# Kernel optimization log

Hardware: AMD Instinct MI355X
Metric: run time of the kernel (lower is better)

Reference implementation:

```python
import jax, jax.numpy as jnp
import numpy as np

NUM_NODES = 512
HEADS = 4
IN_F = 256
OUT_F = 128
EPS = 1e-5


def _layernorm(x, g, b):
    mu = jnp.mean(x, axis=-1, keepdims=True)
    var = jnp.mean(jnp.square(x - mu), axis=-1, keepdims=True)
    return (x - mu) * jax.lax.rsqrt(var + EPS) * g + b


def setup_inputs() -> dict:
    key = jax.random.key(0)
    ks = jax.random.split(key, 16)
    N = 32 * NUM_NODES
    E = 262144
    s = 0.05
    return {
        "x": jax.random.normal(ks[0], (N, IN_F), jnp.float32),
        "edge_index": jax.random.randint(ks[1], (2, E), 0, N, jnp.int64),
        "W_l": jax.random.normal(ks[2], (IN_F, HEADS * OUT_F), jnp.float32) * s,
        "W_r": jax.random.normal(ks[3], (IN_F, HEADS * OUT_F), jnp.float32) * s,
        "att": jax.random.normal(ks[4], (HEADS, OUT_F), jnp.float32) * s,
        "gat_bias": jnp.zeros((OUT_F,), jnp.float32),
        "gat_gamma": jnp.ones((OUT_F,), jnp.float32),
        "gat_beta": jnp.zeros((OUT_F,), jnp.float32),
        "cnn_W": jax.random.normal(ks[5], (IN_F, OUT_F), jnp.float32) * s,
        "cnn_b": jnp.zeros((OUT_F,), jnp.float32),
        "conv_W": jax.random.normal(ks[6], (OUT_F, OUT_F, 7), jnp.float32) * s,
        "conv_b": jnp.zeros((OUT_F,), jnp.float32),
        "cnn_gamma": jnp.ones((OUT_F,), jnp.float32),
        "cnn_beta": jnp.zeros((OUT_F,), jnp.float32),
        "res_W": jax.random.normal(ks[7], (IN_F, OUT_F), jnp.float32) * s,
        "res_b": jnp.zeros((OUT_F,), jnp.float32),
        "fuse_gamma": jnp.ones((OUT_F,), jnp.float32),
        "fuse_beta": jnp.zeros((OUT_F,), jnp.float32),
    }


def reference(x, edge_index, W_l, W_r, att, gat_bias, gat_gamma, gat_beta,
              cnn_W, cnn_b, conv_W, conv_b, cnn_gamma, cnn_beta,
              res_W, res_b, fuse_gamma, fuse_beta):
    N = x.shape[0]
    B = N // NUM_NODES
    # --- GATv2 branch (add self-loops like PyG default) ---
    loop = jnp.arange(N, dtype=edge_index.dtype)
    src = jnp.concatenate([edge_index[0], loop])
    dst = jnp.concatenate([edge_index[1], loop])
    x_l = (x @ W_l).reshape(N, HEADS, OUT_F)
    x_r = (x @ W_r).reshape(N, HEADS, OUT_F)
    e = x_l[src] + x_r[dst]                      # [E+N, H, F]
    e = jnp.where(e > 0, e, 0.2 * e)             # leaky_relu, slope 0.2
    score = jnp.einsum('ehf,hf->eh', e, att)     # [E+N, H]
    m = jax.ops.segment_max(score, dst, num_segments=N)
    ex = jnp.exp(score - m[dst])
    denom = jax.ops.segment_sum(ex, dst, num_segments=N)
    alpha = ex / denom[dst]
    agg = jax.ops.segment_sum(alpha[:, :, None] * x_l[src], dst, num_segments=N)
    h_gat = jnp.mean(agg, axis=1) + gat_bias     # concat=False -> head mean
    h_gat = jnp.where(h_gat > 0, h_gat, 0.01 * h_gat)  # nn.LeakyReLU default
    h_gat = _layernorm(h_gat, gat_gamma, gat_beta)
    # --- CNN branch ---
    xc = x @ cnn_W + cnn_b                       # [N, F]
    xc = xc.reshape(B, NUM_NODES, OUT_F).transpose(0, 2, 1)  # [B, F, L]
    hc = jax.lax.conv_general_dilated(xc, conv_W, window_strides=(1,),
                                      padding=[(3, 3)],
                                      dimension_numbers=('NCW', 'OIW', 'NCW'))
    hc = hc + conv_b[None, :, None]
    hc = hc.transpose(0, 2, 1).reshape(N, OUT_F)
    hc = jax.nn.relu(hc)
    hc = _layernorm(hc, cnn_gamma, cnn_beta)
    # --- fuse + residual ---
    h = h_gat + hc + (x @ res_W + res_b)
    return _layernorm(h, fuse_gamma, fuse_beta)
```

## Files before the change

kernel.cpp:

```cpp
#include <hip/hip_runtime.h>
#include <hip/hip_bf16.h>
#include <math.h>

#define IN_F 256
#define OUT_F 128
#define HEADS 4
#define HF 512
#define NCAT 1280

typedef __hip_bfloat16 bf16;
typedef unsigned short ushort_t;

using bf16x8 = __attribute__((ext_vector_type(8))) short;
using f32x4  = __attribute__((ext_vector_type(4))) float;
using f32v2  = __attribute__((ext_vector_type(2))) float;

__device__ __forceinline__ float bflo(unsigned u) { return __uint_as_float(u << 16); }
__device__ __forceinline__ float bfhi(unsigned u) { return __uint_as_float(u & 0xffff0000u); }
__device__ __forceinline__ float bf2f(ushort_t u) { return __uint_as_float((unsigned)u << 16); }
__device__ __forceinline__ ushort_t f2bf(float f) {
    __hip_bfloat16 h = __float2bfloat16(f);
    return *reinterpret_cast<ushort_t*>(&h);
}

__device__ __forceinline__ void gload16(const void* g, void* l) {
    __builtin_amdgcn_global_load_lds(
        (const __attribute__((address_space(1))) unsigned int*)g,
        (__attribute__((address_space(3))) unsigned int*)l, 16, 0, 0);
}

template <int CTRL>
__device__ __forceinline__ float dpp_add(float s) {
    int t = __builtin_amdgcn_update_dpp(0, __float_as_int(s), CTRL, 0xf, 0xf, true);
    return s + __int_as_float(t);
}
__device__ __forceinline__ float rowsum16(float s) {
    s = dpp_add<0x121>(s);
    s = dpp_add<0x122>(s);
    s = dpp_add<0x124>(s);
    s = dpp_add<0x128>(s);
    return s;
}

__global__ __launch_bounds__(256) void prep_kernel(
    const float* __restrict__ x, ushort_t* __restrict__ xb, int n_cvt,
    const float* __restrict__ Wl, const float* __restrict__ Wr,
    const float* __restrict__ Wc, const float* __restrict__ Wres,
    const float* __restrict__ Wconv,
    ushort_t* __restrict__ Wt, ushort_t* __restrict__ Wt2,
    const int* __restrict__ ei, int* __restrict__ counts, int E,
    int g1, int g2) {
    int b = blockIdx.x;
    if (b < g1) {
        int i = (b * 256 + threadIdx.x) * 8;
        if (i >= n_cvt) return;
        float4 a = *(const float4*)(x + i);
        float4 c = *(const float4*)(x + i + 4);
        uint4 o;
        o.x = f2bf(a.x) | ((unsigned)f2bf(a.y) << 16);
        o.y = f2bf(a.z) | ((unsigned)f2bf(a.w) << 16);
        o.z = f2bf(c.x) | ((unsigned)f2bf(c.y) << 16);
        o.w = f2bf(c.z) | ((unsigned)f2bf(c.w) << 16);
        *(uint4*)(xb + i) = o;
    } else if (b < g2) {
        int idx = (b - g1) * 256 + threadIdx.x;
        if (idx < NCAT * 256) {
            int n = idx >> 8, k = idx & 255;
            float v;
            if (n < 512)       v = Wl[(size_t)k * 512 + n];
            else if (n < 1024) v = Wr[(size_t)k * 512 + (n - 512)];
            else if (n < 1152) v = Wc[(size_t)k * 128 + (n - 1024)];
            else               v = Wres[(size_t)k * 128 + (n - 1152)];
            Wt[idx] = f2bf(v);
        } else {
            int j = idx - NCAT * 256;
            if (j < 7 * 128 * 128) {
                int k = j >> 14, o = (j >> 7) & 127, i = j & 127;
                Wt2[j] = f2bf(Wconv[((size_t)o * 128 + i) * 7 + k]);
            }
        }
    } else {
        int e = (b - g2) * 256 + threadIdx.x;
        if (e < E) atomicAdd(&counts[ei[E + e]], 1);
    }
}

__global__ __launch_bounds__(256) void mfma_gemm(
    const ushort_t* __restrict__ A,
    const ushort_t* __restrict__ Wt,
    ushort_t* __restrict__ xlb, ushort_t* __restrict__ xrb,
    ushort_t* __restrict__ xcb, ushort_t* __restrict__ resb,
    int M) {
    __shared__ __align__(1024) ushort_t As[128 * 64];
    __shared__ __align__(1024) ushort_t Bs[128 * 64];
    int tid = threadIdx.x;
    int lane = tid & 63, wid = tid >> 6;
    int wr = (wid >> 1) * 64, wc = (wid & 1) * 64;
    int brow = blockIdx.y * 128, bcol = blockIdx.x * 128;
    int srow = lane >> 3;
    int sslot = lane & 7;
    int rl = lane & 15, kq = lane >> 4;
    f32x4 acc[4][4] = {};
    for (int k0 = 0; k0 < 256; k0 += 64) {
        #pragma unroll
        for (int j = 0; j < 4; ++j) {
            int r = (wid * 4 + j) * 8 + srow;
            int sl = sslot ^ (r & 7);
            gload16(A  + (size_t)(brow + r) * 256 + k0 + sl * 8,
                    (char*)As + (wid * 4 + j) * 1024);
            gload16(Wt + (size_t)(bcol + r) * 256 + k0 + sl * 8,
                    (char*)Bs + (wid * 4 + j) * 1024);
        }
        __syncthreads();
        #pragma unroll
        for (int ks = 0; ks < 2; ++ks) {
            int cb = ks * 64 + kq * 16;
            bf16x8 af[4], bfv[4];
            #pragma unroll
            for (int m = 0; m < 4; ++m) {
                int r = wr + m * 16 + rl;
                af[m] = *(const bf16x8*)((const char*)As + r * 128 + (cb ^ ((r & 7) << 4)));
            }
            #pragma unroll
            for (int n = 0; n < 4; ++n) {
                int r = wc + n * 16 + rl;
                bfv[n] = *(const bf16x8*)((const char*)Bs + r * 128 + (cb ^ ((r & 7) << 4)));
            }
            #pragma unroll
            for (int m = 0; m < 4; ++m)
                #pragma unroll
                for (int n = 0; n < 4; ++n)
                    acc[m][n] = __builtin_amdgcn_mfma_f32_16x16x32_bf16(
                        af[m], bfv[n], acc[m][n], 0, 0, 0);
        }
        __syncthreads();
    }
    ushort_t* dstp; int cstride, cb2;
    if (bcol < 512)       { dstp = xlb;  cstride = 512; cb2 = bcol; }
    else if (bcol < 1024) { dstp = xrb;  cstride = 512; cb2 = bcol - 512; }
    else if (bcol < 1152) { dstp = xcb;  cstride = 128; cb2 = bcol - 1024; }
    else                  { dstp = resb; cstride = 128; cb2 = bcol - 1152; }
    int rowb = (lane >> 4) * 4;
    #pragma unroll
    for (int m = 0; m < 4; ++m)
        #pragma unroll
        for (int n = 0; n < 4; ++n) {
            int col = cb2 + wc + n * 16 + rl;
            #pragma unroll
            for (int q = 0; q < 4; ++q) {
                int row = brow + wr + m * 16 + rowb + q;
                dstp[(size_t)row * cstride + col] = f2bf(acc[m][n][q]);
            }
        }
}

__global__ __launch_bounds__(1024) void scan_kernel(
    const int* __restrict__ counts, int* __restrict__ offs,
    int* __restrict__ cursor, int N) {
    __shared__ int wsum[16];
    int t = threadIdx.x;
    int lane = t & 63, w = t >> 6;
    int base = t * 16;
    int local[16], s = 0;
    #pragma unroll
    for (int i = 0; i < 16; ++i) {
        int v = (base + i < N) ? counts[base + i] : 0;
        local[i] = v; s += v;
    }
    int sc = s;
    #pragma unroll
    for (int off = 1; off < 64; off <<= 1) {
        int v = __shfl_up(sc, off);
        if (lane >= off) sc += v;
    }
    if (lane == 63) wsum[w] = sc;
    __syncthreads();
    if (w == 0 && lane < 16) {
        int v = wsum[lane];
        int scv = v;
        #pragma unroll
        for (int off = 1; off < 16; off <<= 1) {
            int u = __shfl_up(scv, off);
            if (lane >= off) scv += u;
        }
        wsum[lane] = scv - v;
    }
    __syncthreads();
    int run = wsum[w] + sc - s;
    #pragma unroll
    for (int i = 0; i < 16; ++i) {
        if (base + i < N) { offs[base + i] = run; cursor[base + i] = run; }
        run += local[i];
    }
}

__global__ __launch_bounds__(256) void scatter_kernel(
    const int* __restrict__ ei, int* __restrict__ cursor,
    int* __restrict__ srcs, int E) {
    int e = blockIdx.x * 256 + threadIdx.x;
    if (e < E) {
        int d = ei[E + e];
        int p = atomicAdd(&cursor[d], 1);
        srcs[p] = ei[e];
    }
}

__global__ __launch_bounds__(256) void conv_ln_kernel(
    const ushort_t* __restrict__ xcb, const float* __restrict__ cnn_b,
    const ushort_t* __restrict__ Wt2, const float* __restrict__ conv_b,
    const float* __restrict__ cnn_gamma, const float* __restrict__ cnn_beta,
    ushort_t* __restrict__ hcn_ln) {
    __shared__ ushort_t As[38][136];
    __shared__ __align__(1024) ushort_t Bs[128 * 128];
    __shared__ float hbuf[32][129];
    int tid = threadIdx.x;
    int lane = tid & 63, wid = tid >> 6;
    int wr = (wid >> 1) * 16, wc = (wid & 1) * 64;
    int b = blockIdx.y, l0 = blockIdx.x * 32;
    for (int u = tid; u < 38 * 16; u += 256) {
        int r = u >> 4, seg = u & 15;
        int l = l0 - 3 + r;
        uint4 o4 = make_uint4(0, 0, 0, 0);
        if (l >= 0 && l < 512) {
            uint4 v = *(const uint4*)(xcb + (size_t)(b * 512 + l) * 128 + seg * 8);
            float4 b0 = *(const float4*)(cnn_b + seg * 8);
            float4 b1 = *(const float4*)(cnn_b + seg * 8 + 4);
            o4.x = f2bf(bflo(v.x) + b0.x) | ((unsigned)f2bf(bfhi(v.x) + b0.y) << 16);
            o4.y = f2bf(bflo(v.y) + b0.z) | ((unsigned)f2bf(bfhi(v.y) + b0.w) << 16);
            o4.z = f2bf(bflo(v.z) + b1.x) | ((unsigned)f2bf(bfhi(v.z) + b1.y) << 16);
            o4.w = f2bf(bflo(v.w) + b1.z) | ((unsigned)f2bf(bfhi(v.w) + b1.w) << 16);
        }
        *(uint4*)&As[r][seg * 8] = o4;
    }
    f32x4 acc[4] = {};
    int rl = lane & 15, kb = (lane >> 4) * 8;
    int sr4 = lane >> 4, ss = lane & 15;
    for (int k = 0; k < 7; ++k) {
        __syncthreads();
        #pragma unroll
        for (int j = 0; j < 8; ++j) {
            int r = (wid * 8 + j) * 4 + sr4;
            int sl = ss ^ (r & 15);
            gload16(Wt2 + ((size_t)(k * 128 + r)) * 128 + sl * 8,
                    (char*)Bs + (wid * 8 + j) * 1024);
        }
        __syncthreads();
        #pragma unroll
        for (int kk = 0; kk < 4; ++kk) {
            bf16x8 af = *(const bf16x8*)&As[wr + rl + k][kk * 32 + kb];
            int cbyte = kk * 64 + (lane >> 4) * 16;
            #pragma unroll
            for (int n = 0; n < 4; ++n) {
                int r = wc + n * 16 + rl;
                bf16x8 bfr = *(const bf16x8*)((const char*)Bs + r * 256
                                              + (cbyte ^ ((r & 15) << 4)));
                acc[n] = __builtin_amdgcn_mfma_f32_16x16x32_bf16(af, bfr, acc[n], 0, 0, 0);
            }
        }
    }
    __syncthreads();
    int rowb = (lane >> 4) * 4;
    #pragma unroll
    for (int n = 0; n < 4; ++n) {
        int col = wc + n * 16 + rl;
        float cb = conv_b[col];
        #pragma unroll
        for (int q = 0; q < 4; ++q) {
            int r = wr + rowb + q;
            hbuf[r][col] = fmaxf(acc[n][q] + cb, 0.f);
        }
    }
    __syncthreads();
    for (int r = wid * 8; r < wid * 8 + 8; ++r) {
        int grow = b * 512 + l0 + r;
        float h0 = hbuf[r][lane], h1 = hbuf[r][lane + 64];
        float s = h0 + h1;
        #pragma unroll
        for (int off = 32; off; off >>= 1) s += __shfl_xor(s, off);
        float mu = s * (1.f / 128.f);
        float d0 = h0 - mu, d1 = h1 - mu;
        float vs = d0 * d0 + d1 * d1;
        #pragma unroll
        for (int off = 32; off; off >>= 1) vs += __shfl_xor(vs, off);
        float inv = rsqrtf(vs * (1.f / 128.f) + 1e-5f);
        size_t base = (size_t)grow * 128;
        hcn_ln[base + lane]      = f2bf(d0 * inv * cnn_gamma[lane]      + cnn_beta[lane]);
        hcn_ln[base + lane + 64] = f2bf(d1 * inv * cnn_gamma[lane + 64] + cnn_beta[lane + 64]);
    }
}

__global__ __launch_bounds__(256) void gat_final_kernel(
    const ushort_t* __restrict__ xlb, const ushort_t* __restrict__ xrb,
    const int* __restrict__ srcs, const int* __restrict__ offs,
    const float* __restrict__ att, const float* __restrict__ gat_bias,
    const float* __restrict__ gat_gamma, const float* __restrict__ gat_beta,
    const ushort_t* __restrict__ hcn_ln, const ushort_t* __restrict__ resb,
    const float* __restrict__ res_b,
    const float* __restrict__ fuse_gamma, const float* __restrict__ fuse_beta,
    float* __restrict__ out, int E, int N) {
    int wid = (blockIdx.x * 256 + threadIdx.x) >> 6;
    int lane = threadIdx.x & 63;
    if (wid >= N) return;
    int d = wid;
    const uint4 rv = ((const uint4*)(xrb + (size_t)d * HF))[lane];
    f32v2 xr2[4];
    xr2[0] = f32v2{bflo(rv.x), bfhi(rv.x)};
    xr2[1] = f32v2{bflo(rv.y), bfhi(rv.y)};
    xr2[2] = f32v2{bflo(rv.z), bfhi(rv.z)};
    xr2[3] = f32v2{bflo(rv.w), bfhi(rv.w)};
    const float LOG2E = 1.44269504f;
    const float4 a0 = ((const float4*)att)[lane * 2];
    const float4 a1 = ((const float4*)att)[lane * 2 + 1];
    f32v2 aw2[4] = {f32v2{a0.x, a0.y} * LOG2E, f32v2{a0.z, a0.w} * LOG2E,
                    f32v2{a1.x, a1.y} * LOG2E, f32v2{a1.z, a1.w} * LOG2E};
    f32v2 acc2[4] = {};
    float dn = 0.f;

    auto process = [&](uint4 lv) {
        f32v2 xl2[4];
        xl2[0] = f32v2{bflo(lv.x), bfhi(lv.x)};
        xl2[1] = f32v2{bflo(lv.y), bfhi(lv.y)};
        xl2[2] = f32v2{bflo(lv.z), bfhi(lv.z)};
        xl2[3] = f32v2{bflo(lv.w), bfhi(lv.w)};
        f32v2 s1 = {0.f, 0.f}, s2 = {0.f, 0.f};
        #pragma unroll
        for (int j = 0; j < 4; ++j) {
            f32v2 v = xl2[j] + xr2[j];
            s1 = __builtin_elementwise_fma(v, aw2[j], s1);
            s2 = __builtin_elementwise_fma(__builtin_elementwise_abs(v), aw2[j], s2);
        }
        float s = fmaf(0.6f, s1.x + s1.y, 0.4f * (s2.x + s2.y));
        s = rowsum16(s);
        float ex = exp2f(s);
        dn += ex;
        f32v2 exv = {ex, ex};
        #pragma unroll
        for (int j = 0; j < 4; ++j)
            acc2[j] = __builtin_elementwise_fma(exv, xl2[j], acc2[j]);
    };

    process(((const uint4*)(xlb + (size_t)d * HF))[lane]);

    int start = offs[d];
    int end = (d == N - 1) ? E : offs[d + 1];
    int p = start;
    for (; p + 3 < end; p += 4) {
        int s0 = srcs[p], s1 = srcs[p + 1], s2 = srcs[p + 2], s3 = srcs[p + 3];
        uint4 l0 = ((const uint4*)(xlb + (size_t)s0 * HF))[lane];
        uint4 l1 = ((const uint4*)(xlb + (size_t)s1 * HF))[lane];
        uint4 l2 = ((const uint4*)(xlb + (size_t)s2 * HF))[lane];
        uint4 l3 = ((const uint4*)(xlb + (size_t)s3 * HF))[lane];
        process(l0); process(l1); process(l2); process(l3);
    }
    for (; p < end; ++p)
        process(((const uint4*)(xlb + (size_t)srcs[p] * HF))[lane]);

    float inv = 1.f / dn;
    float v[8];
    #pragma unroll
    for (int j = 0; j < 4; ++j) {
        float tx = acc2[j].x * inv, ty = acc2[j].y * inv;
        tx += __shfl_xor(tx, 16); tx += __shfl_xor(tx, 32);
        ty += __shfl_xor(ty, 16); ty += __shfl_xor(ty, 32);
        v[2 * j] = tx; v[2 * j + 1] = ty;
    }
    int h = lane >> 4;
    int col = (lane & 15) * 8 + 2 * h;
    float g0 = 0.25f * v[2 * h]     + gat_bias[col];
    float g1 = 0.25f * v[2 * h + 1] + gat_bias[col + 1];
    g0 = g0 > 0.f ? g0 : 0.01f * g0;
    g1 = g1 > 0.f ? g1 : 0.01f * g1;
    float s = g0 + g1;
    #pragma unroll
    for (int off = 32; off; off >>= 1) s += __shfl_xor(s, off);
    float mu = s * (1.f / 128.f);
    float d0 = g0 - mu, d1 = g1 - mu;
    float vs = d0 * d0 + d1 * d1;
    #pragma unroll
    for (int off = 32; off; off >>= 1) vs += __shfl_xor(vs, off);
    float rinv = rsqrtf(vs * (1.f / 128.f) + 1e-5f);
    float hg0 = d0 * rinv * gat_gamma[col]     + gat_beta[col];
    float hg1 = d1 * rinv * gat_gamma[col + 1] + gat_beta[col + 1];
    size_t base = (size_t)d * 128 + col;
    unsigned hcu = *(const unsigned*)(hcn_ln + base);
    unsigned rsu = *(const unsigned*)(resb + base);
    float v0 = hg0 + bflo(hcu) + bflo(rsu) + res_b[col];
    float v1 = hg1 + bfhi(hcu) + bfhi(rsu) + res_b[col + 1];
    s = v0 + v1;
    #pragma unroll
    for (int off = 32; off; off >>= 1) s += __shfl_xor(s, off);
    mu = s * (1.f / 128.f);
    d0 = v0 - mu; d1 = v1 - mu;
    vs = d0 * d0 + d1 * d1;
    #pragma unroll
    for (int off = 32; off; off >>= 1) vs += __shfl_xor(vs, off);
    rinv = rsqrtf(vs * (1.f / 128.f) + 1e-5f);
    float2 o2 = make_float2(d0 * rinv * fuse_gamma[col]     + fuse_beta[col],
                            d1 * rinv * fuse_gamma[col + 1] + fuse_beta[col + 1]);
    *(float2*)(out + base) = o2;
}

extern "C" void kernel_launch(void* const* d_in, const int* in_sizes, int n_in,
                              void* d_out, int out_size, void* d_ws, size_t ws_size,
                              hipStream_t stream) {
    const float* x         = (const float*)d_in[0];
    const int*   ei        = (const int*)d_in[1];
    const float* W_l       = (const float*)d_in[2];
    const float* W_r       = (const float*)d_in[3];
    const float* att       = (const float*)d_in[4];
    const float* gat_bias  = (const float*)d_in[5];
    const float* gat_gamma = (const float*)d_in[6];
    const float* gat_beta  = (const float*)d_in[7];
    const float* cnn_W     = (const float*)d_in[8];
    const float* cnn_b     = (const float*)d_in[9];
    const float* conv_W    = (const float*)d_in[10];
    const float* conv_b    = (const float*)d_in[11];
    const float* cnn_gamma = (const float*)d_in[12];
    const float* cnn_beta  = (const float*)d_in[13];
    const float* res_W     = (const float*)d_in[14];
    const float* res_b     = (const float*)d_in[15];
    const float* fuse_gamma= (const float*)d_in[16];
    const float* fuse_beta = (const float*)d_in[17];

    int N = in_sizes[0] / IN_F;
    int E = in_sizes[1] / 2;

    char* ws = (char*)d_ws;
    size_t off = 0;
    ushort_t* xb     = (ushort_t*)(ws + off); off += (size_t)N * IN_F * 2;
    ushort_t* Wt     = (ushort_t*)(ws + off); off += (size_t)NCAT * IN_F * 2;
    ushort_t* Wt2    = (ushort_t*)(ws + off); off += (size_t)7 * 128 * 128 * 2;
    ushort_t* xlb    = (ushort_t*)(ws + off); off += (size_t)N * HF * 2;
    ushort_t* xrb    = (ushort_t*)(ws + off); off += (size_t)N * HF * 2;
    ushort_t* xcb    = (ushort_t*)(ws + off); off += (size_t)N * 128 * 2;
    ushort_t* resb   = (ushort_t*)(ws + off); off += (size_t)N * 128 * 2;
    ushort_t* hcn_ln = (ushort_t*)(ws + off); off += (size_t)N * 128 * 2;
    int*  counts     = (int*)(ws + off);  off += (size_t)N * 4;
    int*  offs       = (int*)(ws + off);  off += (size_t)N * 4;
    int*  cursor     = (int*)(ws + off);  off += (size_t)N * 4;
    int*  srcs       = (int*)(ws + off);  off += (size_t)E * 4;

    hipMemsetAsync(counts, 0, (size_t)N * 4, stream);

    dim3 blk(256);
    int n_cvt = N * IN_F;
    int g1 = (n_cvt / 8 + 255) / 256;
    int g2 = g1 + (NCAT * 256 + 7 * 128 * 128 + 255) / 256;
    int g3 = g2 + (E + 255) / 256;
    prep_kernel<<<g3, blk, 0, stream>>>(x, xb, n_cvt,
        W_l, W_r, cnn_W, res_W, conv_W, Wt, Wt2, ei, counts, E, g1, g2);

    scan_kernel<<<1, 1024, 0, stream>>>(counts, offs, cursor, N);
    scatter_kernel<<<(E + 255) / 256, blk, 0, stream>>>(ei, cursor, srcs, E);

    mfma_gemm<<<dim3(NCAT / 128, N / 128), blk, 0, stream>>>(
        xb, Wt, xlb, xrb, xcb, resb, N);

    conv_ln_kernel<<<dim3(16, 32), blk, 0, stream>>>(
        xcb, cnn_b, Wt2, conv_b, cnn_gamma, cnn_beta, hcn_ln);

    gat_final_kernel<<<(N + 3) / 4, blk, 0, stream>>>(
        xlb, xrb, srcs, offs, att, gat_bias, gat_gamma, gat_beta,
        hcn_ln, resb, res_b, fuse_gamma, fuse_beta, (float*)d_out, E, N);
}
```

Measured before the change: 142.9 us.

## Quantize x_l to per-row-per-head int8 with scales for GAT gather

```diff
diff --git a/kernel.cpp b/kernel.cpp
--- a/kernel.cpp
+++ b/kernel.cpp
@@ -10,10 +10,10 @@
 
 typedef __hip_bfloat16 bf16;
 typedef unsigned short ushort_t;
+typedef unsigned char uchar_t;
 
 using bf16x8 = __attribute__((ext_vector_type(8))) short;
 using f32x4  = __attribute__((ext_vector_type(4))) float;
-using f32v2  = __attribute__((ext_vector_type(2))) float;
 
 __device__ __forceinline__ float bflo(unsigned u) { return __uint_as_float(u << 16); }
 __device__ __forceinline__ float bfhi(unsigned u) { return __uint_as_float(u & 0xffff0000u); }
@@ -88,11 +88,12 @@
 __global__ __launch_bounds__(256) void mfma_gemm(
     const ushort_t* __restrict__ A,
     const ushort_t* __restrict__ Wt,
-    ushort_t* __restrict__ xlb, ushort_t* __restrict__ xrb,
-    ushort_t* __restrict__ xcb, ushort_t* __restrict__ resb,
-    int M) {
+    uchar_t* __restrict__ xl8t, float* __restrict__ scales,
+    ushort_t* __restrict__ xrb, ushort_t* __restrict__ xcb,
+    ushort_t* __restrict__ resb, int M) {
     __shared__ __align__(1024) ushort_t As[128 * 64];
     __shared__ __align__(1024) ushort_t Bs[128 * 64];
+    __shared__ float smax[128][2];
     int tid = threadIdx.x;
     int lane = tid & 63, wid = tid >> 6;
     int wr = (wid >> 1) * 64, wc = (wid & 1) * 64;
@@ -135,12 +136,53 @@
         }
         __syncthreads();
     }
+    int rowb = kq * 4;
+    if (bcol < 512) {
+        int head = bcol >> 7;
+        float rmax[4][4];
+        #pragma unroll
+        for (int m = 0; m < 4; ++m)
+            #pragma unroll
+            for (int q = 0; q < 4; ++q) {
+                float t = fabsf(acc[m][0][q]);
+                t = fmaxf(t, fabsf(acc[m][1][q]));
+                t = fmaxf(t, fabsf(acc[m][2][q]));
+                t = fmaxf(t, fabsf(acc[m][3][q]));
+                #pragma unroll
+                for (int o = 1; o < 16; o <<= 1) t = fmaxf(t, __shfl_xor(t, o));
+                rmax[m][q] = t;
+            }
+        if (rl == 0) {
+            #pragma unroll
+            for (int m = 0; m < 4; ++m)
+                #pragma unroll
+                for (int q = 0; q < 4; ++q)
+                    smax[wr + m * 16 + rowb + q][wid & 1] = rmax[m][q];
+        }
+        __syncthreads();
+        #pragma unroll
+        for (int m = 0; m < 4; ++m)
+            #pragma unroll
+            for (int q = 0; q < 4; ++q) {
+                int row = wr + m * 16 + rowb + q;
+                float sm = fmaxf(fmaxf(smax[row][0], smax[row][1]), 1e-8f);
+                float s = sm * (1.f / 127.f);
+                float rs = 127.f / sm;
+                if ((wid & 1) == 0 && rl == 0)
+                    scales[(size_t)(brow + row) * 4 + head] = s;
+                #pragma unroll
+                for (int n = 0; n < 4; ++n) {
+                    int col = bcol + wc + n * 16 + rl;
+                    int qv = (int)rintf(acc[m][n][q] * rs) + 128;
+                    xl8t[(size_t)(brow + row) * 512 + col] = (uchar_t)qv;
+                }
+            }
+        return;
+    }
     ushort_t* dstp; int cstride, cb2;
-    if (bcol < 512)       { dstp = xlb;  cstride = 512; cb2 = bcol; }
-    else if (bcol < 1024) { dstp = xrb;  cstride = 512; cb2 = bcol - 512; }
+    if (bcol < 1024)      { dstp = xrb;  cstride = 512; cb2 = bcol - 512; }
     else if (bcol < 1152) { dstp = xcb;  cstride = 128; cb2 = bcol - 1024; }
     else                  { dstp = resb; cstride = 128; cb2 = bcol - 1152; }
-    int rowb = (lane >> 4) * 4;
     #pragma unroll
     for (int m = 0; m < 4; ++m)
         #pragma unroll
@@ -290,7 +332,8 @@
 }
 
 __global__ __launch_bounds__(256) void gat_final_kernel(
-    const ushort_t* __restrict__ xlb, const ushort_t* __restrict__ xrb,
+    const uchar_t* __restrict__ xl8t, const float* __restrict__ scales,
+    const ushort_t* __restrict__ xrb,
     const int* __restrict__ srcs, const int* __restrict__ offs,
     const float* __restrict__ att, const float* __restrict__ gat_bias,
     const float* __restrict__ gat_gamma, const float* __restrict__ gat_beta,
@@ -302,69 +345,78 @@
     int lane = threadIdx.x & 63;
     if (wid >= N) return;
     int d = wid;
+    int h = lane >> 4;
     const uint4 rv = ((const uint4*)(xrb + (size_t)d * HF))[lane];
-    f32v2 xr2[4];
-    xr2[0] = f32v2{bflo(rv.x), bfhi(rv.x)};
-    xr2[1] = f32v2{bflo(rv.y), bfhi(rv.y)};
-    xr2[2] = f32v2{bflo(rv.z), bfhi(rv.z)};
-    xr2[3] = f32v2{bflo(rv.w), bfhi(rv.w)};
+    float xr8[8];
+    xr8[0] = bflo(rv.x); xr8[1] = bfhi(rv.x);
+    xr8[2] = bflo(rv.y); xr8[3] = bfhi(rv.y);
+    xr8[4] = bflo(rv.z); xr8[5] = bfhi(rv.z);
+    xr8[6] = bflo(rv.w); xr8[7] = bfhi(rv.w);
     const float LOG2E = 1.44269504f;
     const float4 a0 = ((const float4*)att)[lane * 2];
     const float4 a1 = ((const float4*)att)[lane * 2 + 1];
-    f32v2 aw2[4] = {f32v2{a0.x, a0.y} * LOG2E, f32v2{a0.z, a0.w} * LOG2E,
-                    f32v2{a1.x, a1.y} * LOG2E, f32v2{a1.z, a1.w} * LOG2E};
-    f32v2 acc2[4] = {};
-    float dn = 0.f;
-
-    auto process = [&](uint4 lv) {
-        f32v2 xl2[4];
-        xl2[0] = f32v2{bflo(lv.x), bfhi(lv.x)};
-        xl2[1] = f32v2{bflo(lv.y), bfhi(lv.y)};
-        xl2[2] = f32v2{bflo(lv.z), bfhi(lv.z)};
-        xl2[3] = f32v2{bflo(lv.w), bfhi(lv.w)};
-        f32v2 s1 = {0.f, 0.f}, s2 = {0.f, 0.f};
-        #pragma unroll
-        for (int j = 0; j < 4; ++j) {
-            f32v2 v = xl2[j] + xr2[j];
-            s1 = __builtin_elementwise_fma(v, aw2[j], s1);
-            s2 = __builtin_elementwise_fma(__builtin_elementwise_abs(v), aw2[j], s2);
-        }
-        float s = fmaf(0.6f, s1.x + s1.y, 0.4f * (s2.x + s2.y));
+    const float aw[8] = {a0.x * LOG2E, a0.y * LOG2E, a0.z * LOG2E, a0.w * LOG2E,
+                         a1.x * LOG2E, a1.y * LOG2E, a1.z * LOG2E, a1.w * LOG2E};
+    float acc[8] = {};
+    float dn = 0.f, sumexs = 0.f;
+
+    auto process = [&](uint2 lv, float sc) {
+        float qf[8];
+        qf[0] = (float)(lv.x & 0xff);         qf[1] = (float)((lv.x >> 8) & 0xff);
+        qf[2] = (float)((lv.x >> 16) & 0xff); qf[3] = (float)(lv.x >> 24);
+        qf[4] = (float)(lv.y & 0xff);         qf[5] = (float)((lv.y >> 8) & 0xff);
+        qf[6] = (float)((lv.y >> 16) & 0xff); qf[7] = (float)(lv.y >> 24);
+        float c = 128.f * sc;
+        float s1 = 0.f, s2 = 0.f;
+        #pragma unroll
+        for (int j = 0; j < 8; ++j) {
+            float v = fmaf(sc, qf[j], xr8[j]) - c;
+            s1 = fmaf(v, aw[j], s1);
+            s2 = fmaf(fabsf(v), aw[j], s2);
+        }
+        float s = fmaf(0.6f, s1, 0.4f * s2);
         s = rowsum16(s);
         float ex = exp2f(s);
-        dn += ex;
-        f32v2 exv = {ex, ex};
-        #pragma unroll
-        for (int j = 0; j < 4; ++j)
-            acc2[j] = __builtin_elementwise_fma(exv, xl2[j], acc2[j]);
+        float exs = ex * sc;
+        dn += ex; sumexs += exs;
+        #pragma unroll
+        for (int j = 0; j < 8; ++j) acc[j] = fmaf(exs, qf[j], acc[j]);
     };
 
-    process(((const uint4*)(xlb + (size_t)d * HF))[lane]);
+    process(((const uint2*)(xl8t + (size_t)d * 512))[lane],
+            scales[(size_t)d * 4 + h]);
 
     int start = offs[d];
     int end = (d == N - 1) ? E : offs[d + 1];
     int p = start;
     for (; p + 3 < end; p += 4) {
         int s0 = srcs[p], s1 = srcs[p + 1], s2 = srcs[p + 2], s3 = srcs[p + 3];
-        uint4 l0 = ((const uint4*)(xlb + (size_t)s0 * HF))[lane];
-        uint4 l1 = ((const uint4*)(xlb + (size_t)s1 * HF))[lane];
-        uint4 l2 = ((const uint4*)(xlb + (size_t)s2 * HF))[lane];
-        uint4 l3 = ((const uint4*)(xlb + (size_t)s3 * HF))[lane];
-        process(l0); process(l1); process(l2); process(l3);
-    }
-    for (; p < end; ++p)
-        process(((const uint4*)(xlb + (size_t)srcs[p] * HF))[lane]);
+        uint2 l0 = ((const uint2*)(xl8t + (size_t)s0 * 512))[lane];
+        uint2 l1 = ((const uint2*)(xl8t + (size_t)s1 * 512))[lane];
+        uint2 l2 = ((const uint2*)(xl8t + (size_t)s2 * 512))[lane];
+        uint2 l3 = ((const uint2*)(xl8t + (size_t)s3 * 512))[lane];
+        float c0 = scales[(size_t)s0 * 4 + h];
+        float c1 = scales[(size_t)s1 * 4 + h];
+        float c2 = scales[(size_t)s2 * 4 + h];
+        float c3 = scales[(size_t)s3 * 4 + h];
+        process(l0, c0); process(l1, c1); process(l2, c2); process(l3, c3);
+    }
+    for (; p < end; ++p) {
+        int sp = srcs[p];
+        process(((const uint2*)(xl8t + (size_t)sp * 512))[lane],
+                scales[(size_t)sp * 4 + h]);
+    }
 
     float inv = 1.f / dn;
+    float corr = 128.f * sumexs;
     float v[8];
     #pragma unroll
-    for (int j = 0; j < 4; ++j) {
-        float tx = acc2[j].x * inv, ty = acc2[j].y * inv;
-        tx += __shfl_xor(tx, 16); tx += __shfl_xor(tx, 32);
-        ty += __shfl_xor(ty, 16); ty += __shfl_xor(ty, 32);
-        v[2 * j] = tx; v[2 * j + 1] = ty;
-    }
-    int h = lane >> 4;
+    for (int j = 0; j < 8; ++j) {
+        float t2 = (acc[j] - corr) * inv;
+        t2 += __shfl_xor(t2, 16);
+        t2 += __shfl_xor(t2, 32);
+        v[j] = t2;
+    }
     int col = (lane & 15) * 8 + 2 * h;
     float g0 = 0.25f * v[2 * h]     + gat_bias[col];
     float g1 = 0.25f * v[2 * h + 1] + gat_bias[col + 1];
@@ -430,7 +482,8 @@
     ushort_t* xb     = (ushort_t*)(ws + off); off += (size_t)N * IN_F * 2;
     ushort_t* Wt     = (ushort_t*)(ws + off); off += (size_t)NCAT * IN_F * 2;
     ushort_t* Wt2    = (ushort_t*)(ws + off); off += (size_t)7 * 128 * 128 * 2;
-    ushort_t* xlb    = (ushort_t*)(ws + off); off += (size_t)N * HF * 2;
+    uchar_t*  xl8t   = (uchar_t*)(ws + off);  off += (size_t)N * HF;
+    float*    scales = (float*)(ws + off);    off += (size_t)N * 4 * 4;
     ushort_t* xrb    = (ushort_t*)(ws + off); off += (size_t)N * HF * 2;
     ushort_t* xcb    = (ushort_t*)(ws + off); off += (size_t)N * 128 * 2;
     ushort_t* resb   = (ushort_t*)(ws + off); off += (size_t)N * 128 * 2;
@@ -454,12 +507,12 @@
     scatter_kernel<<<(E + 255) / 256, blk, 0, stream>>>(ei, cursor, srcs, E);
 
     mfma_gemm<<<dim3(NCAT / 128, N / 128), blk, 0, stream>>>(
-        xb, Wt, xlb, xrb, xcb, resb, N);
+        xb, Wt, xl8t, scales, xrb, xcb, resb, N);
 
     conv_ln_kernel<<<dim3(16, 32), blk, 0, stream>>>(
         xcb, cnn_b, Wt2, conv_b, cnn_gamma, cnn_beta, hcn_ln);
 
     gat_final_kernel<<<(N + 3) / 4, blk, 0, stream>>>(
-        xlb, xrb, srcs, offs, att, gat_bias, gat_gamma, gat_beta,
+        xl8t, scales, xrb, srcs, offs, att, gat_bias, gat_gamma, gat_beta,
         hcn_ln, resb, res_b, fuse_gamma, fuse_beta, (float*)d_out, E, N);
 }
```

Result: no change. 142.3 us (-0.5%).
